# Optimization experiments

Hardware: AMD Instinct MI355X
Metric: run time of the kernel (lower is better)

The kernel has to match this reference:

```python
import jax, jax.numpy as jnp
import numpy as np
from jax import lax

EPS = 1e-12  # torch F.normalize eps


def _l2norm(x):
    n = jnp.linalg.norm(x, axis=-1, keepdims=True)
    return x / jnp.maximum(n, EPS)


def _conv1x1(x, w):
    # x: [B,C,H,W], w: [O,C] (1x1 conv, no bias)
    return jnp.einsum('bchw,oc->bohw', x, w)


def _se(x, w1, w2):
    # AdaptiveAvgPool2d(1) -> 1x1 conv (no bias) -> ReLU -> 1x1 conv (no bias) -> ReLU
    p = jnp.mean(x, axis=(2, 3))                      # [B,256]
    h = jax.nn.relu(jnp.einsum('bc,oc->bo', p, w1))   # [B,320]
    return jax.nn.relu(jnp.einsum('bc,oc->bo', h, w2))  # [B,1280]


def _tdec(x, wk_w, wk_b, wv_w, wv_b, red_w, rise_w, rise_b):
    # fc_reduce: 1x1 conv 256->128
    x1 = _conv1x1(x, red_w)                           # [B,128,H,W]
    B, d, H, W = x1.shape
    t = x1.reshape(B, d, H * W).transpose(0, 2, 1)    # [B,N,128] tokens
    # same WK linear produces both q and k (xq == xk in the source)
    k = _l2norm(jnp.einsum('bnd,ed->bne', t, wk_w) + wk_b)  # [B,N,128]
    v = _l2norm(jnp.einsum('bnd,ed->bne', t, wv_w) + wv_b)  # [B,N,128]
    # bmm(wq[B,d,N], wk[B,N,d]) -> [B,d,d] channel gram, temp 30 softmax
    attn = jax.nn.softmax(jnp.einsum('bni,bnj->bij', k, k) * 30.0, axis=-1)
    # bmm(attn[B,d,d], v^T[B,d,N]) -> [B,d,N], reshape back to map
    ot = jnp.einsum('bij,bnj->bin', attn, v).reshape(B, d, H, W)
    return _conv1x1(ot, rise_w) + rise_b[None, :, None, None]


def _fwd(x0, x1, x2, x3, x4, spec_w1, spec_w2, comm_w1, comm_w2,
         pre_w, pre_b, wk1_w, wk1_b, wv1_w, wv1_b, red1_w, rise1_w, rise1_b,
         wk2_w, wk2_b, wv2_w, wv2_b, red2_w, rise2_w, rise2_b):
    xs = jnp.stack([x0, x1, x2, x3, x4])              # [5,B,256,H,W]
    B = x0.shape[0]
    # reduce(lambda x,y: abs(x-y), down_x)
    diff = x0
    for xi in (x1, x2, x3, x4):
        diff = jnp.abs(diff - xi)
    ssum = xs.sum(axis=0)
    wd = jax.nn.softmax(_se(diff, spec_w1, spec_w2).reshape(B, 5, 256), axis=1)
    ws = jax.nn.softmax(_se(ssum, comm_w1, comm_w2).reshape(B, 5, 256), axis=1)
    # v2[i] = x_i*wd_i + x_i*ws_i + x_i ; v3 = sum_i v2[i]
    v3 = jnp.einsum('sbchw,bsc->bchw', xs, wd + ws + 1.0)
    pre = jax.nn.relu(
        lax.conv_general_dilated(v3, pre_w, (1, 1), ((1, 1), (1, 1)),
                                 dimension_numbers=('NCHW', 'OIHW', 'NCHW'))
        + pre_b[None, :, None, None])
    f1 = _tdec(pre, wk1_w, wk1_b, wv1_w, wv1_b, red1_w, rise1_w, rise1_b)
    f3 = _tdec(f1 + v3, wk2_w, wk2_b, wv2_w, wv2_b, red2_w, rise2_w, rise2_b)
    return f1 + f3 + v3


def setup_inputs() -> dict:
    key = jax.random.key(0)
    ks = iter(jax.random.split(key, 40))
    B, C, H, W = 16, 256, 64, 64

    def p(shape, scale=0.05):
        return jax.random.normal(next(ks), shape, jnp.float32) * scale

    inp = {f'x{i}': jax.random.normal(next(ks), (B, C, H, W), jnp.float32) for i in range(5)}
    inp.update(
        spec_w1=p((320, 256)), spec_w2=p((1280, 320)),
        comm_w1=p((320, 256)), comm_w2=p((1280, 320)),
        pre_w=p((256, 256, 3, 3)), pre_b=p((256,)),
        wk1_w=p((128, 128)), wk1_b=p((128,)), wv1_w=p((128, 128)), wv1_b=p((128,)),
        red1_w=p((128, 256)), rise1_w=p((256, 128)), rise1_b=p((256,)),
        wk2_w=p((128, 128)), wk2_b=p((128,)), wv2_w=p((128, 128)), wv2_b=p((128,)),
        red2_w=p((128, 256)), rise2_w=p((256, 128)), rise2_b=p((256,)),
    )
    return inp


def reference(x0, x1, x2, x3, x4, spec_w1, spec_w2, comm_w1, comm_w2,
              pre_w, pre_b, wk1_w, wk1_b, wv1_w, wv1_b, red1_w, rise1_w, rise1_b,
              wk2_w, wk2_b, wv2_w, wv2_b, red2_w, rise2_w, rise2_b):
    return _fwd(x0, x1, x2, x3, x4, spec_w1, spec_w2, comm_w1, comm_w2,
                pre_w, pre_b, wk1_w, wk1_b, wv1_w, wv1_b, red1_w, rise1_w, rise1_b,
                wk2_w, wk2_b, wv2_w, wv2_b, red2_w, rise2_w, rise2_b)
```

## Files before the change

kernel.cpp:

```cpp
#include <hip/hip_runtime.h>

#define DI __device__ __forceinline__

typedef short s16x8 __attribute__((ext_vector_type(8)));
typedef unsigned short u16;
typedef u16 u16x8 __attribute__((ext_vector_type(8)));
typedef u16 u16x16 __attribute__((ext_vector_type(16)));
typedef float f32x4 __attribute__((ext_vector_type(4)));

DI float bf2f(u16 v) { return __builtin_bit_cast(float, (unsigned)v << 16); }
DI u16 f2bf(float f) {
  unsigned u = __builtin_bit_cast(unsigned, f);
  return (u16)((u + 0x7fffu + ((u >> 16) & 1u)) >> 16);
}

__global__ void k_cast(u16* __restrict__ dst, const float* __restrict__ src, int n) {
  int i = blockIdx.x * 256 + threadIdx.x;
  if (i < n) dst[i] = f2bf(src[i]);
}

__global__ void k_wconv(u16* __restrict__ dst, const float* __restrict__ src) {
  int i = blockIdx.x * 256 + threadIdx.x;
  if (i < 9 * 256 * 256) {
    int tap = i >> 16, rem = i & 65535;
    dst[i] = f2bf(src[(size_t)rem * 9 + tap]);
  }
}

__global__ __launch_bounds__(256) void k_pool(
    const float* __restrict__ x0, const float* __restrict__ x1,
    const float* __restrict__ x2, const float* __restrict__ x3,
    const float* __restrict__ x4, float* __restrict__ pd, float* __restrict__ ps) {
  int c = blockIdx.x, b = blockIdx.y;
  size_t base = ((size_t)b * 256 + c) * 4096;
  float sd = 0.f, sm = 0.f;
  for (int p = threadIdx.x; p < 4096; p += 256) {
    float a0 = x0[base + p], a1 = x1[base + p], a2 = x2[base + p];
    float a3 = x3[base + p], a4 = x4[base + p];
    float d = fabsf(a0 - a1); d = fabsf(d - a2); d = fabsf(d - a3); d = fabsf(d - a4);
    sd += d; sm += a0 + a1 + a2 + a3 + a4;
  }
  for (int o = 32; o; o >>= 1) { sd += __shfl_xor(sd, o); sm += __shfl_xor(sm, o); }
  __shared__ float rb[4][2];
  int wv = threadIdx.x >> 6, lane = threadIdx.x & 63;
  if (!lane) { rb[wv][0] = sd; rb[wv][1] = sm; }
  __syncthreads();
  if (!threadIdx.x) {
    float a = rb[0][0] + rb[1][0] + rb[2][0] + rb[3][0];
    float s2 = rb[0][1] + rb[1][1] + rb[2][1] + rb[3][1];
    pd[b * 256 + c] = a * (1.f / 4096.f);
    ps[b * 256 + c] = s2 * (1.f / 4096.f);
  }
}

__global__ __launch_bounds__(256) void k_se1(
    const float* __restrict__ pd, const float* __restrict__ ps,
    const float* __restrict__ sw1, const float* __restrict__ cw1,
    float* __restrict__ h1) {
  int b = blockIdx.y, z = blockIdx.z;
  int wv = threadIdx.x >> 6, lane = threadIdx.x & 63;
  int e = blockIdx.x * 4 + wv;
  const float* in = (z ? ps : pd) + b * 256;
  const float* w = (z ? cw1 : sw1) + (size_t)e * 256;
  float a = 0.f;
#pragma unroll
  for (int i = 0; i < 4; ++i) a += in[lane + 64 * i] * w[lane + 64 * i];
  for (int o = 32; o; o >>= 1) a += __shfl_xor(a, o);
  if (!lane) h1[((size_t)z * 16 + b) * 320 + e] = fmaxf(a, 0.f);
}

__global__ __launch_bounds__(256) void k_se2(
    const float* __restrict__ h1, const float* __restrict__ sw2,
    const float* __restrict__ cw2, float* __restrict__ h2) {
  int b = blockIdx.y, z = blockIdx.z;
  int wv = threadIdx.x >> 6, lane = threadIdx.x & 63;
  int e = blockIdx.x * 4 + wv;
  const float* in = h1 + ((size_t)z * 16 + b) * 320;
  const float* w = (z ? cw2 : sw2) + (size_t)e * 320;
  float a = 0.f;
#pragma unroll
  for (int i = 0; i < 5; ++i) a += in[lane + 64 * i] * w[lane + 64 * i];
  for (int o = 32; o; o >>= 1) a += __shfl_xor(a, o);
  if (!lane) h2[((size_t)z * 16 + b) * 1280 + e] = fmaxf(a, 0.f);
}

__global__ __launch_bounds__(256) void k_se3(
    const float* __restrict__ h2, float* __restrict__ wt) {
  int b = blockIdx.x, t = threadIdx.x;
  const float* Hs = h2 + (size_t)b * 1280;
  const float* Hc = h2 + (size_t)(16 + b) * 1280;
  float d0 = Hs[t], d1 = Hs[256 + t], d2 = Hs[512 + t], d3 = Hs[768 + t], d4 = Hs[1024 + t];
  float m = fmaxf(fmaxf(fmaxf(d0, d1), fmaxf(d2, d3)), d4);
  float e0 = expf(d0 - m), e1 = expf(d1 - m), e2 = expf(d2 - m), e3 = expf(d3 - m), e4 = expf(d4 - m);
  float inv = 1.f / (e0 + e1 + e2 + e3 + e4);
  float c0 = Hc[t], c1 = Hc[256 + t], c2 = Hc[512 + t], c3 = Hc[768 + t], c4 = Hc[1024 + t];
  float mc = fmaxf(fmaxf(fmaxf(c0, c1), fmaxf(c2, c3)), c4);
  float g0 = expf(c0 - mc), g1 = expf(c1 - mc), g2 = expf(c2 - mc), g3 = expf(c3 - mc), g4 = expf(c4 - mc);
  float ci = 1.f / (g0 + g1 + g2 + g3 + g4);
  size_t base = (size_t)b * 1280 + t;
  wt[base + 0 * 256] = e0 * inv + g0 * ci + 1.f;
  wt[base + 1 * 256] = e1 * inv + g1 * ci + 1.f;
  wt[base + 2 * 256] = e2 * inv + g2 * ci + 1.f;
  wt[base + 3 * 256] = e3 * inv + g3 * ci + 1.f;
  wt[base + 4 * 256] = e4 * inv + g4 * ci + 1.f;
}

__global__ __launch_bounds__(256) void k_v3(
    const float* __restrict__ x0, const float* __restrict__ x1,
    const float* __restrict__ x2, const float* __restrict__ x3,
    const float* __restrict__ x4, const float* __restrict__ wt,
    u16* __restrict__ v3b) {
  int h = blockIdx.x, b = blockIdx.y;
  __shared__ float W[1280];
  for (int s = threadIdx.x; s < 1280; s += 256) W[s] = wt[(size_t)b * 1280 + s];
  __syncthreads();
  int t = threadIdx.x, w = t >> 2, oct = t & 3;
  size_t pbase = ((size_t)b * 256) * 4096 + h * 64 + w;
  size_t obase = ((size_t)b * 4096 + h * 64 + w) * 256;
  for (int pass = 0; pass < 8; ++pass) {
    int c0 = oct * 8 + pass * 32;
    u16x8 ov;
#pragma unroll
    for (int jj = 0; jj < 8; ++jj) {
      int c = c0 + jj;
      size_t a = pbase + (size_t)c * 4096;
      float s = x0[a] * W[c] + x1[a] * W[256 + c] + x2[a] * W[512 + c] +
                x3[a] * W[768 + c] + x4[a] * W[1024 + c];
      ov[jj] = f2bf(s);
    }
    *(u16x8*)(v3b + obase + c0) = ov;
  }
}

__global__ __launch_bounds__(256) void k_conv(
    const u16* __restrict__ v3b, const u16* __restrict__ Wt,
    const float* __restrict__ bias, u16* __restrict__ pre) {
  int o = blockIdx.x;
  int wg = (o & 7) * 128 + (o >> 3);
  int oh = wg & 1, hp = (wg >> 1) & 31, b = wg >> 6;
  __shared__ __align__(16) u16 Ain[4 * 66 * 40];
  __shared__ __align__(16) u16 Bld[2][128 * 40];
  int t = threadIdx.x, wv = t >> 6, lane = t & 63;
  int wm = (wv >> 1) * 64, wn = (wv & 1) * 64, fr = lane & 15, ko = lane >> 4;

  auto loadA = [&](int cc, int s) -> u16x16 {
    int r = s >> 7, rest = s & 127, w = rest >> 1, half = rest & 1;
    int hs = hp * 2 - 1 + r;
    u16x16 v = {};
    if ((unsigned)hs < 64u)
      v = *(const u16x16*)(v3b + (((size_t)b * 64 + hs) * 64 + w) * 256 + cc * 32 + half * 16);
    return v;
  };
  auto storeA = [&](int s, u16x16 v) {
    int r = s >> 7, rest = s & 127, w = rest >> 1, half = rest & 1;
    *(u16x16*)(Ain + (r * 66 + w + 1) * 40 + half * 16) = v;
  };
  auto loadB = [&](int tap, int cc) -> u16x16 {
    int n = t >> 1, half = t & 1;
    return *(const u16x16*)(Wt + ((size_t)tap * 256 + oh * 128 + n) * 256 + cc * 32 + half * 16);
  };
  auto storeB = [&](int bsel, u16x16 v) {
    int n = t >> 1, half = t & 1;
    *(u16x16*)(Bld[bsel] + n * 40 + half * 16) = v;
  };

  for (int s = t; s < 320; s += 256) {
    int r = s / 80, rem = s % 80;
    int col = (rem >= 40) ? 65 : 0, c = rem % 40;
    Ain[(r * 66 + col) * 40 + c] = 0;
  }
  storeA(t, loadA(0, t));
  storeA(t + 256, loadA(0, t + 256));
  storeB(0, loadB(0, 0));
  __syncthreads();

  f32x4 acc[4][4] = {};
  int buf = 0;
  for (int cc = 0; cc < 8; ++cc) {
#pragma unroll
    for (int tap = 0; tap < 9; ++tap) {
      u16x16 pA0, pA1, pB;
      bool doA = false, doB = false;
      if (tap < 8) {
        doB = true;
        pB = loadB(tap + 1, cc);
      } else if (cc < 7) {
        doA = true; doB = true;
        pB = loadB(0, cc + 1);
        pA0 = loadA(cc + 1, t);
        pA1 = loadA(cc + 1, t + 256);
      }
      const int dh = tap / 3 - 1, dw = tap % 3 - 1;
      s16x8 af[4], bfr[4];
#pragma unroll
      for (int i = 0; i < 4; ++i) {
        int m = wm + i * 16 + fr, r = m >> 6, wq = m & 63;
        af[i] = *(const s16x8*)(Ain + ((r + dh + 1) * 66 + (wq + dw + 1)) * 40 + ko * 8);
      }
#pragma unroll
      for (int j = 0; j < 4; ++j)
        bfr[j] = *(const s16x8*)(Bld[buf] + (wn + j * 16 + fr) * 40 + ko * 8);
#pragma unroll
      for (int i = 0; i < 4; ++i)
#pragma unroll
        for (int j = 0; j < 4; ++j)
          acc[i][j] = __builtin_amdgcn_mfma_f32_16x16x32_bf16(af[i], bfr[j], acc[i][j], 0, 0, 0);
      if (doA) __syncthreads();
      if (doB) storeB(buf ^ 1, pB);
      if (doA) { storeA(t, pA0); storeA(t + 256, pA1); }
      __syncthreads();
      buf ^= 1;
    }
  }
#pragma unroll
  for (int i = 0; i < 4; ++i) {
    int m0 = wm + i * 16 + ko * 4;
#pragma unroll
    for (int j = 0; j < 4; ++j) {
      int och = oh * 128 + wn + j * 16 + fr;
      float bv = bias[och];
#pragma unroll
      for (int r = 0; r < 4; ++r) {
        float v = fmaxf(acc[i][j][r] + bv, 0.f);
        pre[((size_t)b * 4096 + hp * 128 + m0 + r) * 256 + och] = f2bf(v);
      }
    }
  }
}

template <int MODE>
__global__ __launch_bounds__(256) void k_gemm(
    const u16* __restrict__ A, int lda, const u16* __restrict__ B0,
    const u16* __restrict__ B1, int ldb, int K,
    const float* __restrict__ bias0, const float* __restrict__ bias1,
    u16* __restrict__ out0, u16* __restrict__ out1,
    const u16* __restrict__ add0, const u16* __restrict__ add1,
    float* __restrict__ outf) {
  int nt = blockIdx.x, b = blockIdx.y, z = blockIdx.z;
  const u16* Ab = A + ((size_t)b * 4096 + nt * 128) * (size_t)lda;
  const u16* Bb;
  if constexpr (MODE == 1) Bb = (z ? B1 : B0);
  else if constexpr (MODE == 2) Bb = B0 + (size_t)b * 128 * ldb;
  else Bb = B0 + (size_t)z * 128 * ldb;
  __shared__ __align__(16) u16 Ald[128 * 40];
  __shared__ __align__(16) u16 Bld[128 * 40];
  int t = threadIdx.x, wv = t >> 6, lane = t & 63;
  int wm = (wv >> 1) * 64, wn = (wv & 1) * 64, fr = lane & 15, ko = lane >> 4;
  f32x4 acc[4][4] = {};
  for (int kc = 0; kc < K; kc += 32) {
    for (int s = t; s < 512; s += 256) {
      int r = s >> 2, ks = s & 3;
      *(u16x8*)(Ald + r * 40 + ks * 8) = *(const u16x8*)(Ab + (size_t)r * lda + kc + ks * 8);
    }
    for (int s = t; s < 512; s += 256) {
      int r = s >> 2, ks = s & 3;
      *(u16x8*)(Bld + r * 40 + ks * 8) = *(const u16x8*)(Bb + (size_t)r * ldb + kc + ks * 8);
    }
    __syncthreads();
    s16x8 af[4], bf[4];
#pragma unroll
    for (int i = 0; i < 4; ++i) af[i] = *(const s16x8*)(Ald + (wm + i * 16 + fr) * 40 + ko * 8);
#pragma unroll
    for (int j = 0; j < 4; ++j) bf[j] = *(const s16x8*)(Bld + (wn + j * 16 + fr) * 40 + ko * 8);
#pragma unroll
    for (int i = 0; i < 4; ++i)
#pragma unroll
      for (int j = 0; j < 4; ++j)
        acc[i][j] = __builtin_amdgcn_mfma_f32_16x16x32_bf16(af[i], bf[j], acc[i][j], 0, 0, 0);
    __syncthreads();
  }
  size_t tokbase = (size_t)b * 4096 + nt * 128;
#pragma unroll
  for (int i = 0; i < 4; ++i) {
    int m0 = wm + i * 16 + ko * 4;
#pragma unroll
    for (int j = 0; j < 4; ++j) {
      int nc = wn + j * 16 + fr;
      if constexpr (MODE == 0 || MODE == 2) {
        u16* dst = out0 + (tokbase + m0) * 128 + nc;
#pragma unroll
        for (int r = 0; r < 4; ++r) dst[(size_t)r * 128] = f2bf(acc[i][j][r]);
      } else if constexpr (MODE == 1) {
        float bv = (z ? bias1 : bias0)[nc];
        u16* dst = (z ? out1 : out0) + (tokbase + m0) * 128 + nc;
#pragma unroll
        for (int r = 0; r < 4; ++r) dst[(size_t)r * 128] = f2bf(acc[i][j][r] + bv);
      } else if constexpr (MODE == 3) {
        int o = z * 128 + nc;
        float bv = bias0[o];
        size_t idx = (tokbase + m0) * 256 + o;
#pragma unroll
        for (int r = 0; r < 4; ++r) {
          float f1v = acc[i][j][r] + bv;
          out0[idx + (size_t)r * 256] = f2bf(f1v);
          out1[idx + (size_t)r * 256] = f2bf(f1v + bf2f(add0[idx + (size_t)r * 256]));
        }
      } else {
        int o = z * 128 + nc;
        float bv = bias0[o];
        size_t idx = (tokbase + m0) * 256 + o;
        f32x4 vv;
#pragma unroll
        for (int r = 0; r < 4; ++r)
          vv[r] = acc[i][j][r] + bv + bf2f(add0[idx + (size_t)r * 256]) + bf2f(add1[idx + (size_t)r * 256]);
        *(f32x4*)(outf + ((size_t)b * 256 + o) * 4096 + nt * 128 + m0) = vv;
      }
    }
  }
}

__global__ __launch_bounds__(256) void k_norm(const u16* __restrict__ kraw,
                                              u16* __restrict__ ktout,
                                              u16* __restrict__ vbuf) {
  int nt = blockIdx.x, b = blockIdx.y, kind = blockIdx.z;
  int t = threadIdx.x, r = t >> 2, q = t & 3;
  __shared__ __align__(16) u16 T[128 * 72];
  size_t row = (size_t)b * 4096 + nt * 64 + r;
  const u16* src = (kind ? (const u16*)vbuf : kraw) + row * 128 + q * 32;
  float vals[32];
  float ss = 0.f;
#pragma unroll
  for (int s = 0; s < 4; ++s) {
    u16x8 v8 = *(const u16x8*)(src + s * 8);
#pragma unroll
    for (int e = 0; e < 8; ++e) { float f = bf2f(v8[e]); vals[s * 8 + e] = f; ss += f * f; }
  }
  ss += __shfl_xor(ss, 1);
  ss += __shfl_xor(ss, 2);
  float sc = 1.f / fmaxf(sqrtf(ss), 1e-12f);
  if (kind) {
    u16* dst = vbuf + row * 128 + q * 32;
#pragma unroll
    for (int s = 0; s < 4; ++s) {
      u16x8 o8;
#pragma unroll
      for (int e = 0; e < 8; ++e) o8[e] = f2bf(vals[s * 8 + e] * sc);
      *(u16x8*)(dst + s * 8) = o8;
    }
  } else {
#pragma unroll
    for (int s = 0; s < 4; ++s)
#pragma unroll
      for (int e = 0; e < 8; ++e)
        T[(q * 32 + s * 8 + e) * 72 + r] = f2bf(vals[s * 8 + e] * sc);
    __syncthreads();
    for (int s2 = t; s2 < 1024; s2 += 256) {
      int i = s2 >> 3, sg = s2 & 7;
      *(u16x8*)(ktout + ((size_t)b * 128 + i) * 4096 + nt * 64 + sg * 8) =
          *(const u16x8*)(T + i * 72 + sg * 8);
    }
  }
}

__global__ __launch_bounds__(256) void k_gram(const u16* __restrict__ kt, float* __restrict__ gp) {
  int ks = blockIdx.x, b = blockIdx.y;
  const u16* base = kt + (size_t)b * 128 * 4096 + ks * 256;
  __shared__ __align__(16) u16 Tld[128 * 40];
  int t = threadIdx.x, wv = t >> 6, lane = t & 63;
  int wm = (wv >> 1) * 64, wn = (wv & 1) * 64, fr = lane & 15, ko = lane >> 4;
  f32x4 acc[4][4] = {};
  for (int kc = 0; kc < 256; kc += 32) {
    for (int s = t; s < 512; s += 256) {
      int r = s >> 2, k2 = s & 3;
      *(u16x8*)(Tld + r * 40 + k2 * 8) = *(const u16x8*)(base + (size_t)r * 4096 + kc + k2 * 8);
    }
    __syncthreads();
    s16x8 af[4], bf[4];
#pragma unroll
    for (int i = 0; i < 4; ++i) af[i] = *(const s16x8*)(Tld + (wm + i * 16 + fr) * 40 + ko * 8);
#pragma unroll
    for (int j = 0; j < 4; ++j) bf[j] = *(const s16x8*)(Tld + (wn + j * 16 + fr) * 40 + ko * 8);
#pragma unroll
    for (int i = 0; i < 4; ++i)
#pragma unroll
      for (int j = 0; j < 4; ++j)
        acc[i][j] = __builtin_amdgcn_mfma_f32_16x16x32_bf16(af[i], bf[j], acc[i][j], 0, 0, 0);
    __syncthreads();
  }
  float* dst = gp + ((size_t)(ks * 16 + b) * 128) * 128;
#pragma unroll
  for (int i = 0; i < 4; ++i) {
    int m0 = wm + i * 16 + ko * 4;
#pragma unroll
    for (int j = 0; j < 4; ++j) {
      int nc = wn + j * 16 + fr;
#pragma unroll
      for (int r = 0; r < 4; ++r) dst[(size_t)(m0 + r) * 128 + nc] = acc[i][j][r];
    }
  }
}

__global__ void k_soft(const float* __restrict__ gp, u16* __restrict__ attn) {
  int i = blockIdx.x, b = blockIdx.y, l = threadIdx.x;
  float s0 = 0.f, s1 = 0.f;
  for (int ks = 0; ks < 16; ++ks) {
    const float* row = gp + (((size_t)ks * 16 + b) * 128 + i) * 128;
    s0 += row[l]; s1 += row[l + 64];
  }
  s0 *= 30.f; s1 *= 30.f;
  float m = fmaxf(s0, s1);
  for (int o = 32; o; o >>= 1) m = fmaxf(m, __shfl_xor(m, o));
  float e0 = expf(s0 - m), e1 = expf(s1 - m);
  float s = e0 + e1;
  for (int o = 32; o; o >>= 1) s += __shfl_xor(s, o);
  float inv = 1.f / s;
  u16* dst = attn + ((size_t)b * 128 + i) * 128;
  dst[l] = f2bf(e0 * inv);
  dst[l + 64] = f2bf(e1 * inv);
}

extern "C" void kernel_launch(void* const* d_in, const int* in_sizes, int n_in,
                              void* d_out, int out_size, void* d_ws, size_t ws_size,
                              hipStream_t stream) {
  (void)in_sizes; (void)n_in; (void)out_size; (void)ws_size;
  const float* x0 = (const float*)d_in[0];
  const float* x1 = (const float*)d_in[1];
  const float* x2 = (const float*)d_in[2];
  const float* x3 = (const float*)d_in[3];
  const float* x4 = (const float*)d_in[4];
  const float* spec_w1 = (const float*)d_in[5];
  const float* spec_w2 = (const float*)d_in[6];
  const float* comm_w1 = (const float*)d_in[7];
  const float* comm_w2 = (const float*)d_in[8];
  const float* pre_w = (const float*)d_in[9];
  const float* pre_bias = (const float*)d_in[10];
  const float* wk1_w = (const float*)d_in[11];
  const float* wk1_b = (const float*)d_in[12];
  const float* wv1_w = (const float*)d_in[13];
  const float* wv1_b = (const float*)d_in[14];
  const float* red1_w = (const float*)d_in[15];
  const float* rise1_w = (const float*)d_in[16];
  const float* rise1_b = (const float*)d_in[17];
  const float* wk2_w = (const float*)d_in[18];
  const float* wk2_b = (const float*)d_in[19];
  const float* wv2_w = (const float*)d_in[20];
  const float* wv2_b = (const float*)d_in[21];
  const float* red2_w = (const float*)d_in[22];
  const float* rise2_w = (const float*)d_in[23];
  const float* rise2_b = (const float*)d_in[24];
  float* out = (float*)d_out;

  char* wsp = (char*)d_ws;
  size_t off = 0;
  auto alloc = [&](size_t bytes) -> void* {
    off = (off + 255) & ~(size_t)255;
    void* p = wsp + off;
    off += bytes;
    return p;
  };
  float* pd = (float*)alloc(16 * 256 * 4);
  float* ps = (float*)alloc(16 * 256 * 4);
  float* h1b = (float*)alloc(2 * 16 * 320 * 4);
  float* h2b = (float*)alloc(2 * 16 * 1280 * 4);
  float* wtb = (float*)alloc(16 * 5 * 256 * 4);
  u16* v3b = (u16*)alloc((size_t)16 * 4096 * 256 * 2);
  u16* Wtc = (u16*)alloc((size_t)9 * 256 * 256 * 2);
  u16* red1b = (u16*)alloc(128 * 256 * 2);
  u16* wk1b = (u16*)alloc(128 * 128 * 2);
  u16* wv1b = (u16*)alloc(128 * 128 * 2);
  u16* rise1b = (u16*)alloc(256 * 128 * 2);
  u16* red2b = (u16*)alloc(128 * 256 * 2);
  u16* wk2b = (u16*)alloc(128 * 128 * 2);
  u16* wv2b = (u16*)alloc(128 * 128 * 2);
  u16* rise2b = (u16*)alloc(256 * 128 * 2);
  u16* pre = (u16*)alloc((size_t)16 * 4096 * 256 * 2);
  u16* tbuf = (u16*)alloc((size_t)16 * 4096 * 128 * 2);
  u16* kraw = (u16*)alloc((size_t)16 * 4096 * 128 * 2);
  u16* khat = (u16*)alloc((size_t)16 * 4096 * 128 * 2);
  u16* vbuf = (u16*)alloc((size_t)16 * 4096 * 128 * 2);
  u16* attn = (u16*)alloc((size_t)16 * 128 * 128 * 2);
  u16* Obuf = (u16*)alloc((size_t)16 * 4096 * 128 * 2);
  u16* f1b = (u16*)alloc((size_t)16 * 4096 * 256 * 2);
  float* gpart = (float*)tbuf;
  u16* in2b = pre;

  k_cast<<<dim3(128), 256, 0, stream>>>(red1b, red1_w, 32768);
  k_cast<<<dim3(64), 256, 0, stream>>>(wk1b, wk1_w, 16384);
  k_cast<<<dim3(64), 256, 0, stream>>>(wv1b, wv1_w, 16384);
  k_cast<<<dim3(128), 256, 0, stream>>>(rise1b, rise1_w, 32768);
  k_cast<<<dim3(128), 256, 0, stream>>>(red2b, red2_w, 32768);
  k_cast<<<dim3(64), 256, 0, stream>>>(wk2b, wk2_w, 16384);
  k_cast<<<dim3(64), 256, 0, stream>>>(wv2b, wv2_w, 16384);
  k_cast<<<dim3(128), 256, 0, stream>>>(rise2b, rise2_w, 32768);
  k_wconv<<<dim3(2304), 256, 0, stream>>>(Wtc, pre_w);

  k_pool<<<dim3(256, 16), 256, 0, stream>>>(x0, x1, x2, x3, x4, pd, ps);
  k_se1<<<dim3(80, 16, 2), 256, 0, stream>>>(pd, ps, spec_w1, comm_w1, h1b);
  k_se2<<<dim3(320, 16, 2), 256, 0, stream>>>(h1b, spec_w2, comm_w2, h2b);
  k_se3<<<dim3(16), 256, 0, stream>>>(h2b, wtb);
  k_v3<<<dim3(64, 16), 256, 0, stream>>>(x0, x1, x2, x3, x4, wtb, v3b);
  k_conv<<<dim3(1024), 256, 0, stream>>>(v3b, Wtc, pre_bias, pre);

  k_gemm<0><<<dim3(32, 16, 1), 256, 0, stream>>>(pre, 256, red1b, nullptr, 256, 256,
      nullptr, nullptr, tbuf, nullptr, nullptr, nullptr, nullptr);
  k_gemm<1><<<dim3(32, 16, 2), 256, 0, stream>>>(tbuf, 128, wk1b, wv1b, 128, 128,
      wk1_b, wv1_b, kraw, vbuf, nullptr, nullptr, nullptr);
  k_norm<<<dim3(64, 16, 2), 256, 0, stream>>>(kraw, khat, vbuf);
  k_gram<<<dim3(16, 16), 256, 0, stream>>>(khat, gpart);
  k_soft<<<dim3(128, 16), 64, 0, stream>>>(gpart, attn);
  k_gemm<2><<<dim3(32, 16, 1), 256, 0, stream>>>(vbuf, 128, attn, nullptr, 128, 128,
      nullptr, nullptr, Obuf, nullptr, nullptr, nullptr, nullptr);
  k_gemm<3><<<dim3(32, 16, 2), 256, 0, stream>>>(Obuf, 128, rise1b, nullptr, 128, 128,
      rise1_b, nullptr, f1b, in2b, v3b, nullptr, nullptr);

  k_gemm<0><<<dim3(32, 16, 1), 256, 0, stream>>>(in2b, 256, red2b, nullptr, 256, 256,
      nullptr, nullptr, tbuf, nullptr, nullptr, nullptr, nullptr);
  k_gemm<1><<<dim3(32, 16, 2), 256, 0, stream>>>(tbuf, 128, wk2b, wv2b, 128, 128,
      wk2_b, wv2_b, kraw, vbuf, nullptr, nullptr, nullptr);
  k_norm<<<dim3(64, 16, 2), 256, 0, stream>>>(kraw, khat, vbuf);
  k_gram<<<dim3(16, 16), 256, 0, stream>>>(khat, gpart);
  k_soft<<<dim3(128, 16), 64, 0, stream>>>(gpart, attn);
  k_gemm<2><<<dim3(32, 16, 1), 256, 0, stream>>>(vbuf, 128, attn, nullptr, 128, 128,
      nullptr, nullptr, Obuf, nullptr, nullptr, nullptr, nullptr);
  k_gemm<4><<<dim3(32, 16, 2), 256, 0, stream>>>(Obuf, 128, rise2b, nullptr, 128, 128,
      rise2_b, nullptr, nullptr, nullptr, f1b, v3b, out);
}
```

Before: 536.6 us.

## Coalesce v3 loads via LDS transpose and stage conv weights with global_load_lds

The v3 kernel now reads each input channel row with consecutive lanes on consecutive pixels, so global loads coalesce. Results are transposed through a shared-memory tile before the channel-contiguous bf16 store. The conv kernel loads weight tiles straight into LDS with global_load_lds instead of bouncing through registers, and drops the padded stride. The unpadded 32-element B layout may add LDS bank conflicts, and the correctness of the async loads depends on the existing barriers (no explicit vmcnt wait).

```diff
diff --git a/kernel.cpp b/kernel.cpp
--- a/kernel.cpp
+++ b/kernel.cpp
@@ -112,22 +112,27 @@
     u16* __restrict__ v3b) {
   int h = blockIdx.x, b = blockIdx.y;
   __shared__ float W[1280];
-  for (int s = threadIdx.x; s < 1280; s += 256) W[s] = wt[(size_t)b * 1280 + s];
+  __shared__ u16 T[256][72];
+  int t = threadIdx.x, wv = t >> 6, l = t & 63;
+  for (int s = t; s < 1280; s += 256) W[s] = wt[(size_t)b * 1280 + s];
   __syncthreads();
-  int t = threadIdx.x, w = t >> 2, oct = t & 3;
-  size_t pbase = ((size_t)b * 256) * 4096 + h * 64 + w;
+  size_t rowbase = (size_t)b * 256 * 4096 + h * 64 + l;
+#pragma unroll 4
+  for (int k = 0; k < 64; ++k) {
+    int c = wv * 64 + k;
+    size_t a = rowbase + (size_t)c * 4096;
+    float s = x0[a] * W[c] + x1[a] * W[256 + c] + x2[a] * W[512 + c] +
+              x3[a] * W[768 + c] + x4[a] * W[1024 + c];
+    T[c][l] = f2bf(s);
+  }
+  __syncthreads();
+  int w = t >> 2, oct = t & 3;
   size_t obase = ((size_t)b * 4096 + h * 64 + w) * 256;
   for (int pass = 0; pass < 8; ++pass) {
     int c0 = oct * 8 + pass * 32;
     u16x8 ov;
 #pragma unroll
-    for (int jj = 0; jj < 8; ++jj) {
-      int c = c0 + jj;
-      size_t a = pbase + (size_t)c * 4096;
-      float s = x0[a] * W[c] + x1[a] * W[256 + c] + x2[a] * W[512 + c] +
-                x3[a] * W[768 + c] + x4[a] * W[1024 + c];
-      ov[jj] = f2bf(s);
-    }
+    for (int jj = 0; jj < 8; ++jj) ov[jj] = T[c0 + jj][w];
     *(u16x8*)(v3b + obase + c0) = ov;
   }
 }
@@ -139,7 +144,7 @@
   int wg = (o & 7) * 128 + (o >> 3);
   int oh = wg & 1, hp = (wg >> 1) & 31, b = wg >> 6;
   __shared__ __align__(16) u16 Ain[4 * 66 * 40];
-  __shared__ __align__(16) u16 Bld[2][128 * 40];
+  __shared__ __align__(16) u16 Bls[2][128 * 32];
   int t = threadIdx.x, wv = t >> 6, lane = t & 63;
   int wm = (wv >> 1) * 64, wn = (wv & 1) * 64, fr = lane & 15, ko = lane >> 4;
 
@@ -155,13 +160,16 @@
     int r = s >> 7, rest = s & 127, w = rest >> 1, half = rest & 1;
     *(u16x16*)(Ain + (r * 66 + w + 1) * 40 + half * 16) = v;
   };
-  auto loadB = [&](int tap, int cc) -> u16x16 {
-    int n = t >> 1, half = t & 1;
-    return *(const u16x16*)(Wt + ((size_t)tap * 256 + oh * 128 + n) * 256 + cc * 32 + half * 16);
-  };
-  auto storeB = [&](int bsel, u16x16 v) {
-    int n = t >> 1, half = t & 1;
-    *(u16x16*)(Bld[bsel] + n * 40 + half * 16) = v;
+  auto stageB = [&](int bsel, int tap, int cc) {
+#pragma unroll
+    for (int c = 0; c < 2; ++c) {
+      int n = wv * 32 + c * 16 + (lane >> 2);
+      const u16* g = Wt + ((size_t)tap * 256 + oh * 128 + n) * 256 + cc * 32 + (lane & 3) * 8;
+      __builtin_amdgcn_global_load_lds(
+          (const __attribute__((address_space(1))) void*)g,
+          (__attribute__((address_space(3))) void*)&Bls[bsel][(wv * 32 + c * 16) * 32],
+          16, 0, 0);
+    }
   };
 
   for (int s = t; s < 320; s += 256) {
@@ -169,9 +177,9 @@
     int col = (rem >= 40) ? 65 : 0, c = rem % 40;
     Ain[(r * 66 + col) * 40 + c] = 0;
   }
+  stageB(0, 0, 0);
   storeA(t, loadA(0, t));
   storeA(t + 256, loadA(0, t + 256));
-  storeB(0, loadB(0, 0));
   __syncthreads();
 
   f32x4 acc[4][4] = {};
@@ -179,17 +187,11 @@
   for (int cc = 0; cc < 8; ++cc) {
 #pragma unroll
     for (int tap = 0; tap < 9; ++tap) {
-      u16x16 pA0, pA1, pB;
-      bool doA = false, doB = false;
-      if (tap < 8) {
-        doB = true;
-        pB = loadB(tap + 1, cc);
-      } else if (cc < 7) {
-        doA = true; doB = true;
-        pB = loadB(0, cc + 1);
-        pA0 = loadA(cc + 1, t);
-        pA1 = loadA(cc + 1, t + 256);
-      }
+      if (tap < 8) stageB(buf ^ 1, tap + 1, cc);
+      else if (cc < 7) stageB(buf ^ 1, 0, cc + 1);
+      u16x16 pA0, pA1;
+      const bool doA = (tap == 8 && cc < 7);
+      if (doA) { pA0 = loadA(cc + 1, t); pA1 = loadA(cc + 1, t + 256); }
       const int dh = tap / 3 - 1, dw = tap % 3 - 1;
       s16x8 af[4], bfr[4];
 #pragma unroll
@@ -199,15 +201,17 @@
       }
 #pragma unroll
       for (int j = 0; j < 4; ++j)
-        bfr[j] = *(const s16x8*)(Bld[buf] + (wn + j * 16 + fr) * 40 + ko * 8);
+        bfr[j] = *(const s16x8*)(Bls[buf] + (wn + j * 16 + fr) * 32 + ko * 8);
 #pragma unroll
       for (int i = 0; i < 4; ++i)
 #pragma unroll
         for (int j = 0; j < 4; ++j)
           acc[i][j] = __builtin_amdgcn_mfma_f32_16x16x32_bf16(af[i], bfr[j], acc[i][j], 0, 0, 0);
-      if (doA) __syncthreads();
-      if (doB) storeB(buf ^ 1, pB);
-      if (doA) { storeA(t, pA0); storeA(t + 256, pA1); }
+      if (doA) {
+        __syncthreads();
+        storeA(t, pA0);
+        storeA(t + 256, pA1);
+      }
       __syncthreads();
       buf ^= 1;
     }
```

After: 559.4 us. 4.2% more time.
